# Optimization experiments

Measured on AMD Instinct MI355X. Metric: run time of the kernel, lower is better.

Reference implementation:

```python
import jax, jax.numpy as jnp
import numpy as np

N_NODES = 50000
N_EDGES = 800000
D_IN = 64
D_OUT = 64


def setup_inputs() -> dict:
    key = jax.random.key(0)
    k1, k2, k3, k4, k5 = jax.random.split(key, 5)
    x = jax.random.normal(k1, (N_NODES, D_IN), dtype=jnp.float32)
    senders = jax.random.randint(k2, (N_EDGES,), 0, N_NODES, dtype=jnp.int32)
    receivers = jax.random.randint(k3, (N_EDGES,), 0, N_NODES, dtype=jnp.int32)
    # eqx.nn.Linear params: weight [out, in], bias [out]
    weight = jax.random.normal(k4, (D_OUT, D_IN), dtype=jnp.float32) / np.sqrt(D_IN)
    bias = jax.random.normal(k5, (D_OUT,), dtype=jnp.float32) * 0.01
    return {"x": x, "senders": senders, "receivers": receivers, "weight": weight, "bias": bias}


def reference(x, senders, receivers, weight, bias):
    n = x.shape[0]
    # jraph.GraphConvolution applies update_node_fn (the Linear) FIRST
    h = x @ weight.T + bias  # [N, D_OUT]
    # add self edges
    self_idx = jnp.arange(n, dtype=senders.dtype)
    cs = jnp.concatenate([senders, self_idx])
    cr = jnp.concatenate([receivers, self_idx])
    ones = jnp.ones(cs.shape, dtype=h.dtype)
    sender_deg = jax.ops.segment_sum(ones, cs, num_segments=n)
    receiver_deg = jax.ops.segment_sum(ones, cr, num_segments=n)
    # symmetric normalization: D^{-1/2} A D^{-1/2}
    h = h * jax.lax.rsqrt(jnp.maximum(sender_deg, 1.0))[:, None]
    h = jax.ops.segment_sum(h[cs], cr, num_segments=n)  # gather -> scatter-add
    h = h * jax.lax.rsqrt(jnp.maximum(receiver_deg, 1.0))[:, None]
    return jax.nn.leaky_relu(h)  # default negative_slope=0.01
```

## Files before the change

kernel.cpp:

```cpp
#include <hip/hip_runtime.h>

#define N_NODES 50000
#define N_EDGES 800000
#define D 64
#define NB 196
#define BSZ 256
#define NSLICE 196
#define E4 (N_EDGES / 4)

__device__ __forceinline__ ushort f2bf(float f) {
    unsigned u = __float_as_uint(f);
    unsigned r = u + 0x7fffu + ((u >> 16) & 1u);
    return (ushort)(r >> 16);
}
__device__ __forceinline__ void acc8(const uint4 a, float* acc) {
    acc[0] += __uint_as_float(a.x << 16);
    acc[1] += __uint_as_float(a.x & 0xffff0000u);
    acc[2] += __uint_as_float(a.y << 16);
    acc[3] += __uint_as_float(a.y & 0xffff0000u);
    acc[4] += __uint_as_float(a.z << 16);
    acc[5] += __uint_as_float(a.z & 0xffff0000u);
    acc[6] += __uint_as_float(a.w << 16);
    acc[7] += __uint_as_float(a.w & 0xffff0000u);
}

__global__ __launch_bounds__(1024) void count_kernel(
        const int* __restrict__ s, const int* __restrict__ r,
        int* __restrict__ rcnt, int* __restrict__ scnt) {
    __shared__ int rh[NB], sh[NB];
    const int tid = threadIdx.x, sl = blockIdx.x;
    for (int i = tid; i < NB; i += 1024) { rh[i] = 0; sh[i] = 0; }
    __syncthreads();

    int e4 = sl * 1024 + tid;
    if (e4 < E4) {
        int4 rv = ((const int4*)r)[e4];
        int4 sv = ((const int4*)s)[e4];
        atomicAdd(&rh[rv.x >> 8], 1); atomicAdd(&rh[rv.y >> 8], 1);
        atomicAdd(&rh[rv.z >> 8], 1); atomicAdd(&rh[rv.w >> 8], 1);
        atomicAdd(&sh[sv.x >> 8], 1); atomicAdd(&sh[sv.y >> 8], 1);
        atomicAdd(&sh[sv.z >> 8], 1); atomicAdd(&sh[sv.w >> 8], 1);
    }
    __syncthreads();
    for (int i = tid; i < NB; i += 1024) {
        rcnt[i * NSLICE + sl] = rh[i];
        scnt[i * NSLICE + sl] = sh[i];
    }
}

__global__ __launch_bounds__(256) void scanA_kernel(
        int* __restrict__ rcnt, int* __restrict__ scnt,
        int* __restrict__ rtot, int* __restrict__ stot) {
    __shared__ int sc[256];
    const int tid = threadIdx.x;
    const int b = blockIdx.x;
    int* arr = (b < NB) ? rcnt : scnt;
    int* tot = (b < NB) ? rtot : stot;
    const int bb = (b < NB) ? b : b - NB;

    int v = (tid < NSLICE) ? arr[bb * NSLICE + tid] : 0;
    sc[tid] = v;
    __syncthreads();
    for (int o = 1; o < 256; o <<= 1) {
        int u = (tid >= o) ? sc[tid - o] : 0;
        __syncthreads();
        sc[tid] += u;
        __syncthreads();
    }
    if (tid < NSLICE) arr[bb * NSLICE + tid] = sc[tid] - v;
    if (tid == 255) tot[bb] = sc[255];
}

__global__ __launch_bounds__(1024) void part_kernel(
        const int* __restrict__ s, const int* __restrict__ r,
        const int* __restrict__ rcnt, const int* __restrict__ scnt,
        const int* __restrict__ rtot, const int* __restrict__ stot,
        unsigned* __restrict__ pr, unsigned char* __restrict__ ps8) {
    __shared__ int rcur[NB], scur[NB];
    __shared__ int sc[256];
    const int tid = threadIdx.x, sl = blockIdx.x;

    if (tid < 256) sc[tid] = (tid < NB) ? rtot[tid] : 0;
    __syncthreads();
    for (int o = 1; o < 256; o <<= 1) {
        int u = 0;
        if (tid < 256 && tid >= o) u = sc[tid - o];
        __syncthreads();
        if (tid < 256) sc[tid] += u;
        __syncthreads();
    }
    if (tid < NB) rcur[tid] = ((tid == 0) ? 0 : sc[tid - 1]) + rcnt[tid * NSLICE + sl];
    __syncthreads();
    if (tid < 256) sc[tid] = (tid < NB) ? stot[tid] : 0;
    __syncthreads();
    for (int o = 1; o < 256; o <<= 1) {
        int u = 0;
        if (tid < 256 && tid >= o) u = sc[tid - o];
        __syncthreads();
        if (tid < 256) sc[tid] += u;
        __syncthreads();
    }
    if (tid < NB) scur[tid] = ((tid == 0) ? 0 : sc[tid - 1]) + scnt[tid * NSLICE + sl];
    __syncthreads();

    int e4 = sl * 1024 + tid;
    if (e4 < E4) {
        int4 rv = ((const int4*)r)[e4];
        int4 sv = ((const int4*)s)[e4];
        int ri[4] = {rv.x, rv.y, rv.z, rv.w};
        int si[4] = {sv.x, sv.y, sv.z, sv.w};
        #pragma unroll
        for (int k = 0; k < 4; ++k) {
            int pos = atomicAdd(&rcur[ri[k] >> 8], 1);
            pr[pos] = ((unsigned)(ri[k] & 255) << 16) | (unsigned)si[k];
            int pos2 = atomicAdd(&scur[si[k] >> 8], 1);
            ps8[pos2] = (unsigned char)(si[k] & 255);
        }
    }
}

__global__ __launch_bounds__(256) void post_kernel(
        const unsigned* __restrict__ pr,
        const int* __restrict__ rtot, const int* __restrict__ stot,
        int* __restrict__ rowoff, ushort* __restrict__ csr16,
        const unsigned char* __restrict__ ps8, float* __restrict__ sscale) {
    __shared__ int sc[256];
    const int tid = threadIdx.x;

    if (blockIdx.x >= NB) {
        __shared__ int hist[BSZ];
        const int b = blockIdx.x - NB;
        sc[tid] = (tid < NB) ? stot[tid] : 0;
        __syncthreads();
        for (int o = 1; o < 256; o <<= 1) {
            int u = (tid >= o) ? sc[tid - o] : 0;
            __syncthreads();
            sc[tid] += u;
            __syncthreads();
        }
        const int sb = (b == 0) ? 0 : sc[b - 1];
        const int se = sc[b];
        hist[tid] = 0;
        __syncthreads();
        for (int i = sb + tid; i < se; i += 256) atomicAdd(&hist[ps8[i]], 1);
        __syncthreads();
        int n = b * BSZ + tid;
        if (n < N_NODES) sscale[n] = rsqrtf((float)(hist[tid] + 1));
        return;
    }
    __shared__ int hist2[BSZ];
    __shared__ int cur[BSZ];
    const int b = blockIdx.x;
    sc[tid] = (tid < NB) ? rtot[tid] : 0;
    __syncthreads();
    for (int o = 1; o < 256; o <<= 1) {
        int u = (tid >= o) ? sc[tid - o] : 0;
        __syncthreads();
        sc[tid] += u;
        __syncthreads();
    }
    const int rb = (b == 0) ? 0 : sc[b - 1];
    const int re = sc[b];

    hist2[tid] = 0;
    __syncthreads();
    for (int i = rb + tid; i < re; i += 256)
        atomicAdd(&hist2[pr[i] >> 16], 1);
    __syncthreads();

    int v = hist2[tid];
    __syncthreads();
    hist2[tid] = v;
    __syncthreads();
    for (int o = 1; o < 256; o <<= 1) {
        int u = (tid >= o) ? hist2[tid - o] : 0;
        __syncthreads();
        hist2[tid] += u;
        __syncthreads();
    }
    int excl = hist2[tid] - v;
    int n = b * BSZ + tid;
    if (n < N_NODES) rowoff[n] = rb + excl;
    cur[tid] = rb + excl;
    if (b == NB - 1 && tid == 0) rowoff[N_NODES] = N_EDGES;
    __syncthreads();

    for (int i = rb + tid; i < re; i += 256) {
        unsigned pw = pr[i];
        int pos = atomicAdd(&cur[pw >> 16], 1);
        csr16[pos] = (ushort)(pw & 0xffffu);
    }
}

__global__ __launch_bounds__(256, 4) void linear_kernel(
        const float* __restrict__ x, const float* __restrict__ w,
        const float* __restrict__ bias, const float* __restrict__ sscale,
        ushort* __restrict__ h16) {
    __shared__ float wlds[64 * 68];
    __shared__ float xlds[64 * 68];
    __shared__ float blds[64];
    __shared__ float slds[64];
    const int t = threadIdx.x;
    const int t15 = t & 15;
    const int g = t >> 4;
    const int nb = blockIdx.x * 64;

    #pragma unroll
    for (int q = 0; q < 4; ++q) {
        int idx = q * 256 + t;
        int o = idx >> 4, k4 = idx & 15;
        float4 wv = ((const float4*)w)[idx];
        *(float4*)&wlds[o * 68 + k4 * 4] = wv;
    }
    if (t < 64) {
        blds[t] = bias[t];
        int n = nb + t;
        slds[t] = (n < N_NODES) ? sscale[n] : 0.f;
    }
    #pragma unroll
    for (int q = 0; q < 4; ++q) {
        int idx = q * 256 + t;
        int nl = idx >> 4, k4 = idx & 15;
        int n = nb + nl;
        float4 xv = (n < N_NODES) ? ((const float4*)x)[n * 16 + k4]
                                  : make_float4(0.f, 0.f, 0.f, 0.f);
        *(float4*)&xlds[nl * 68 + k4 * 4] = xv;
    }
    __syncthreads();

    float acc[4][4];
    #pragma unroll
    for (int i = 0; i < 4; ++i)
        #pragma unroll
        for (int j = 0; j < 4; ++j) acc[i][j] = 0.f;

    #pragma unroll 2
    for (int k4 = 0; k4 < 16; ++k4) {
        float4 wv0 = *(const float4*)&wlds[(t15     ) * 68 + k4 * 4];
        float4 wv1 = *(const float4*)&wlds[(t15 + 16) * 68 + k4 * 4];
        float4 wv2 = *(const float4*)&wlds[(t15 + 32) * 68 + k4 * 4];
        float4 wv3 = *(const float4*)&wlds[(t15 + 48) * 68 + k4 * 4];
        #pragma unroll
        for (int i = 0; i < 4; ++i) {
            float4 xv = *(const float4*)&xlds[(g * 4 + i) * 68 + k4 * 4];
            acc[i][0] += xv.x * wv0.x + xv.y * wv0.y + xv.z * wv0.z + xv.w * wv0.w;
            acc[i][1] += xv.x * wv1.x + xv.y * wv1.y + xv.z * wv1.z + xv.w * wv1.w;
            acc[i][2] += xv.x * wv2.x + xv.y * wv2.y + xv.z * wv2.z + xv.w * wv2.w;
            acc[i][3] += xv.x * wv3.x + xv.y * wv3.y + xv.z * wv3.z + xv.w * wv3.w;
        }
    }

    #pragma unroll
    for (int i = 0; i < 4; ++i) {
        int nl = g * 4 + i;
        int n = nb + nl;
        if (n < N_NODES) {
            float sc = slds[nl];
            h16[n * D + t15     ] = f2bf((acc[i][0] + blds[t15     ]) * sc);
            h16[n * D + t15 + 16] = f2bf((acc[i][1] + blds[t15 + 16]) * sc);
            h16[n * D + t15 + 32] = f2bf((acc[i][2] + blds[t15 + 32]) * sc);
            h16[n * D + t15 + 48] = f2bf((acc[i][3] + blds[t15 + 48]) * sc);
        }
    }
}

__global__ __launch_bounds__(256) void gather_kernel(
        const ushort* __restrict__ h16, const int* __restrict__ rowoff,
        const ushort* __restrict__ csr16, float* __restrict__ out) {
    const int lane = threadIdx.x & 63;
    const int q = lane & 7;
    const int g = lane >> 3;
    const int n = blockIdx.x * 4 + (threadIdx.x >> 6);
    if (n >= N_NODES) return;

    float acc[8];
    #pragma unroll
    for (int k = 0; k < 8; ++k) acc[k] = 0.f;

    const int base = rowoff[n];
    const int cnt = rowoff[n + 1] - base;

    for (int j0 = 0; j0 < cnt; j0 += 64) {
        int m = cnt - j0; if (m > 64) m = 64;
        int my = (lane < m) ? (int)csr16[base + j0 + lane] : 0;
        int t = 0;
        for (; t + 16 <= m; t += 16) {
            int s0 = __shfl(my, t + g);
            int s1 = __shfl(my, t + 8 + g);
            uint4 a = *(const uint4*)&h16[s0 * D + q * 8];
            uint4 b = *(const uint4*)&h16[s1 * D + q * 8];
            acc8(a, acc);
            acc8(b, acc);
        }
        for (; t < m; t += 8) {
            int e = t + g;
            int ee = (e < m) ? e : 0;
            int s0 = __shfl(my, ee);
            if (e < m) {
                uint4 a = *(const uint4*)&h16[s0 * D + q * 8];
                acc8(a, acc);
            }
        }
    }

    #pragma unroll
    for (int k = 0; k < 8; ++k) acc[k] += __shfl_xor(acc[k], 8);
    #pragma unroll
    for (int k = 0; k < 8; ++k) acc[k] += __shfl_xor(acc[k], 16);
    #pragma unroll
    for (int k = 0; k < 8; ++k) acc[k] += __shfl_xor(acc[k], 32);

    uint4 sv = *(const uint4*)&h16[n * D + q * 8];
    acc8(sv, acc);
    float sc = rsqrtf((float)(cnt + 1));
    float o[8];
    #pragma unroll
    for (int k = 0; k < 8; ++k) {
        float vv = acc[k] * sc;
        o[k] = vv > 0.f ? vv : 0.01f * vv;
    }
    if (g == 0) {
        float4* op = (float4*)(out + n * D + q * 8);
        op[0] = make_float4(o[0], o[1], o[2], o[3]);
        op[1] = make_float4(o[4], o[5], o[6], o[7]);
    }
}

extern "C" void kernel_launch(void* const* d_in, const int* in_sizes, int n_in,
                              void* d_out, int out_size, void* d_ws, size_t ws_size,
                              hipStream_t stream) {
    const float* x       = (const float*)d_in[0];
    const int*   senders = (const int*)d_in[1];
    const int*   recvs   = (const int*)d_in[2];
    const float* weight  = (const float*)d_in[3];
    const float* bias    = (const float*)d_in[4];
    float* out = (float*)d_out;

    char* p = (char*)d_ws;
    auto take = [&](size_t bytes) { char* q = p; p += (bytes + 255) & ~(size_t)255; return q; };
    ushort*        h16    = (ushort*)take((size_t)N_NODES * D * 2);
    float*         sscale = (float*)take((size_t)N_NODES * 4);
    unsigned*      pr     = (unsigned*)take((size_t)N_EDGES * 4);
    unsigned char* ps8    = (unsigned char*)take((size_t)N_EDGES);
    int*           rcnt   = (int*)take((size_t)NB * NSLICE * 4);
    int*           scnt   = (int*)take((size_t)NB * NSLICE * 4);
    int*           rtot   = (int*)take((size_t)NB * 4);
    int*           stot   = (int*)take((size_t)NB * 4);
    int*           rowoff = (int*)take((size_t)(N_NODES + 1) * 4);
    ushort*        csr16  = (ushort*)take((size_t)N_EDGES * 2);

    hipLaunchKernelGGL(count_kernel, dim3(NSLICE), dim3(1024), 0, stream,
                       senders, recvs, rcnt, scnt);
    hipLaunchKernelGGL(scanA_kernel, dim3(2 * NB), dim3(256), 0, stream,
                       rcnt, scnt, rtot, stot);
    hipLaunchKernelGGL(part_kernel, dim3(NSLICE), dim3(1024), 0, stream,
                       senders, recvs, rcnt, scnt, rtot, stot, pr, ps8);
    hipLaunchKernelGGL(post_kernel, dim3(2 * NB), dim3(BSZ), 0, stream,
                       pr, rtot, stot, rowoff, csr16, ps8, sscale);
    hipLaunchKernelGGL(linear_kernel, dim3((N_NODES + 63) / 64), dim3(256), 0, stream,
                       x, weight, bias, sscale, h16);
    hipLaunchKernelGGL(gather_kernel, dim3((N_NODES + 3) / 4), dim3(256), 0, stream,
                       h16, rowoff, csr16, out);
}
```

Measured before the change: 76.92 us.

## Fuse CSR build kernels into one cooperative kernel with grid syncs

```diff
diff --git a/kernel.cpp b/kernel.cpp
--- a/kernel.cpp
+++ b/kernel.cpp
@@ -1,12 +1,17 @@
 #include <hip/hip_runtime.h>
+#include <hip/hip_cooperative_groups.h>
+
+namespace cg = cooperative_groups;
 
 #define N_NODES 50000
 #define N_EDGES 800000
 #define D 64
 #define NB 196
 #define BSZ 256
-#define NSLICE 196
-#define E4 (N_EDGES / 4)
+#define MBLK 256
+#define MTHR 1024
+#define SLICE_E 3136
+#define SLICE_I4 784
 
 __device__ __forceinline__ ushort f2bf(float f) {
     unsigned u = __float_as_uint(f);
@@ -24,61 +29,70 @@
     acc[7] += __uint_as_float(a.w & 0xffff0000u);
 }
 
-__global__ __launch_bounds__(1024) void count_kernel(
+__global__ __launch_bounds__(MTHR) void mega_kernel(
         const int* __restrict__ s, const int* __restrict__ r,
-        int* __restrict__ rcnt, int* __restrict__ scnt) {
+        int* __restrict__ rcnt, int* __restrict__ scnt,
+        int* __restrict__ rtot, int* __restrict__ stot,
+        unsigned* __restrict__ pr, unsigned char* __restrict__ ps8,
+        int* __restrict__ rowoff, ushort* __restrict__ csr16,
+        float* __restrict__ sscale) {
+    __shared__ unsigned ecache[SLICE_E];
     __shared__ int rh[NB], sh[NB];
-    const int tid = threadIdx.x, sl = blockIdx.x;
-    for (int i = tid; i < NB; i += 1024) { rh[i] = 0; sh[i] = 0; }
-    __syncthreads();
-
-    int e4 = sl * 1024 + tid;
-    if (e4 < E4) {
-        int4 rv = ((const int4*)r)[e4];
-        int4 sv = ((const int4*)s)[e4];
-        atomicAdd(&rh[rv.x >> 8], 1); atomicAdd(&rh[rv.y >> 8], 1);
-        atomicAdd(&rh[rv.z >> 8], 1); atomicAdd(&rh[rv.w >> 8], 1);
-        atomicAdd(&sh[sv.x >> 8], 1); atomicAdd(&sh[sv.y >> 8], 1);
-        atomicAdd(&sh[sv.z >> 8], 1); atomicAdd(&sh[sv.w >> 8], 1);
-    }
-    __syncthreads();
-    for (int i = tid; i < NB; i += 1024) {
-        rcnt[i * NSLICE + sl] = rh[i];
-        scnt[i * NSLICE + sl] = sh[i];
-    }
-}
-
-__global__ __launch_bounds__(256) void scanA_kernel(
-        int* __restrict__ rcnt, int* __restrict__ scnt,
-        int* __restrict__ rtot, int* __restrict__ stot) {
     __shared__ int sc[256];
+    __shared__ int h4[256];
+    __shared__ int c4[256];
+    cg::grid_group grid = cg::this_grid();
+
     const int tid = threadIdx.x;
-    const int b = blockIdx.x;
-    int* arr = (b < NB) ? rcnt : scnt;
-    int* tot = (b < NB) ? rtot : stot;
-    const int bb = (b < NB) ? b : b - NB;
-
-    int v = (tid < NSLICE) ? arr[bb * NSLICE + tid] : 0;
-    sc[tid] = v;
-    __syncthreads();
-    for (int o = 1; o < 256; o <<= 1) {
-        int u = (tid >= o) ? sc[tid - o] : 0;
-        __syncthreads();
-        sc[tid] += u;
-        __syncthreads();
-    }
-    if (tid < NSLICE) arr[bb * NSLICE + tid] = sc[tid] - v;
-    if (tid == 255) tot[bb] = sc[255];
-}
-
-__global__ __launch_bounds__(1024) void part_kernel(
-        const int* __restrict__ s, const int* __restrict__ r,
-        const int* __restrict__ rcnt, const int* __restrict__ scnt,
-        const int* __restrict__ rtot, const int* __restrict__ stot,
-        unsigned* __restrict__ pr, unsigned char* __restrict__ ps8) {
-    __shared__ int rcur[NB], scur[NB];
-    __shared__ int sc[256];
-    const int tid = threadIdx.x, sl = blockIdx.x;
+    const int sl = blockIdx.x;
+    const int ebase = sl * SLICE_E;
+    const int ecount = min(SLICE_E, N_EDGES - ebase);
+    const int i4n = (ecount + 3) >> 2;
+
+    for (int i = tid; i < NB; i += MTHR) { rh[i] = 0; sh[i] = 0; }
+    __syncthreads();
+    if (tid < i4n) {
+        int4 rv = ((const int4*)r)[sl * SLICE_I4 + tid];
+        int4 sv = ((const int4*)s)[sl * SLICE_I4 + tid];
+        int ri[4] = {rv.x, rv.y, rv.z, rv.w};
+        int si[4] = {sv.x, sv.y, sv.z, sv.w};
+        #pragma unroll
+        for (int k = 0; k < 4; ++k) {
+            atomicAdd(&rh[ri[k] >> 8], 1);
+            atomicAdd(&sh[si[k] >> 8], 1);
+            ecache[tid * 4 + k] = ((unsigned)ri[k] << 16) | (unsigned)si[k];
+        }
+    }
+    __syncthreads();
+    for (int i = tid; i < NB; i += MTHR) {
+        rcnt[i * MBLK + sl] = rh[i];
+        scnt[i * MBLK + sl] = sh[i];
+    }
+    grid.sync();
+
+    #pragma unroll
+    for (int jj = 0; jj < 2; ++jj) {
+        int job = sl + jj * MBLK;
+        if (job < 2 * NB) {
+            int* arr = (job < NB) ? rcnt : scnt;
+            int* tot = (job < NB) ? rtot : stot;
+            int bb = (job < NB) ? job : job - NB;
+            int v = 0;
+            if (tid < 256) { v = arr[bb * MBLK + tid]; sc[tid] = v; }
+            __syncthreads();
+            for (int o = 1; o < 256; o <<= 1) {
+                int u = 0;
+                if (tid < 256 && tid >= o) u = sc[tid - o];
+                __syncthreads();
+                if (tid < 256) sc[tid] += u;
+                __syncthreads();
+            }
+            if (tid < 256) arr[bb * MBLK + tid] = sc[tid] - v;
+            if (tid == 255) tot[bb] = sc[255];
+            __syncthreads();
+        }
+    }
+    grid.sync();
 
     if (tid < 256) sc[tid] = (tid < NB) ? rtot[tid] : 0;
     __syncthreads();
@@ -89,7 +103,7 @@
         if (tid < 256) sc[tid] += u;
         __syncthreads();
     }
-    if (tid < NB) rcur[tid] = ((tid == 0) ? 0 : sc[tid - 1]) + rcnt[tid * NSLICE + sl];
+    if (tid < NB) rh[tid] = ((tid == 0) ? 0 : sc[tid - 1]) + rcnt[tid * MBLK + sl];
     __syncthreads();
     if (tid < 256) sc[tid] = (tid < NB) ? stot[tid] : 0;
     __syncthreads();
@@ -100,95 +114,91 @@
         if (tid < 256) sc[tid] += u;
         __syncthreads();
     }
-    if (tid < NB) scur[tid] = ((tid == 0) ? 0 : sc[tid - 1]) + scnt[tid * NSLICE + sl];
-    __syncthreads();
-
-    int e4 = sl * 1024 + tid;
-    if (e4 < E4) {
-        int4 rv = ((const int4*)r)[e4];
-        int4 sv = ((const int4*)s)[e4];
-        int ri[4] = {rv.x, rv.y, rv.z, rv.w};
-        int si[4] = {sv.x, sv.y, sv.z, sv.w};
-        #pragma unroll
-        for (int k = 0; k < 4; ++k) {
-            int pos = atomicAdd(&rcur[ri[k] >> 8], 1);
-            pr[pos] = ((unsigned)(ri[k] & 255) << 16) | (unsigned)si[k];
-            int pos2 = atomicAdd(&scur[si[k] >> 8], 1);
-            ps8[pos2] = (unsigned char)(si[k] & 255);
-        }
-    }
-}
-
-__global__ __launch_bounds__(256) void post_kernel(
-        const unsigned* __restrict__ pr,
-        const int* __restrict__ rtot, const int* __restrict__ stot,
-        int* __restrict__ rowoff, ushort* __restrict__ csr16,
-        const unsigned char* __restrict__ ps8, float* __restrict__ sscale) {
-    __shared__ int sc[256];
-    const int tid = threadIdx.x;
-
-    if (blockIdx.x >= NB) {
-        __shared__ int hist[BSZ];
-        const int b = blockIdx.x - NB;
-        sc[tid] = (tid < NB) ? stot[tid] : 0;
-        __syncthreads();
-        for (int o = 1; o < 256; o <<= 1) {
-            int u = (tid >= o) ? sc[tid - o] : 0;
-            __syncthreads();
-            sc[tid] += u;
-            __syncthreads();
-        }
-        const int sb = (b == 0) ? 0 : sc[b - 1];
-        const int se = sc[b];
-        hist[tid] = 0;
-        __syncthreads();
-        for (int i = sb + tid; i < se; i += 256) atomicAdd(&hist[ps8[i]], 1);
-        __syncthreads();
-        int n = b * BSZ + tid;
-        if (n < N_NODES) sscale[n] = rsqrtf((float)(hist[tid] + 1));
-        return;
-    }
-    __shared__ int hist2[BSZ];
-    __shared__ int cur[BSZ];
-    const int b = blockIdx.x;
-    sc[tid] = (tid < NB) ? rtot[tid] : 0;
-    __syncthreads();
-    for (int o = 1; o < 256; o <<= 1) {
-        int u = (tid >= o) ? sc[tid - o] : 0;
-        __syncthreads();
-        sc[tid] += u;
-        __syncthreads();
-    }
-    const int rb = (b == 0) ? 0 : sc[b - 1];
-    const int re = sc[b];
-
-    hist2[tid] = 0;
-    __syncthreads();
-    for (int i = rb + tid; i < re; i += 256)
-        atomicAdd(&hist2[pr[i] >> 16], 1);
-    __syncthreads();
-
-    int v = hist2[tid];
-    __syncthreads();
-    hist2[tid] = v;
-    __syncthreads();
-    for (int o = 1; o < 256; o <<= 1) {
-        int u = (tid >= o) ? hist2[tid - o] : 0;
-        __syncthreads();
-        hist2[tid] += u;
-        __syncthreads();
-    }
-    int excl = hist2[tid] - v;
-    int n = b * BSZ + tid;
-    if (n < N_NODES) rowoff[n] = rb + excl;
-    cur[tid] = rb + excl;
-    if (b == NB - 1 && tid == 0) rowoff[N_NODES] = N_EDGES;
-    __syncthreads();
-
-    for (int i = rb + tid; i < re; i += 256) {
-        unsigned pw = pr[i];
-        int pos = atomicAdd(&cur[pw >> 16], 1);
-        csr16[pos] = (ushort)(pw & 0xffffu);
+    if (tid < NB) sh[tid] = ((tid == 0) ? 0 : sc[tid - 1]) + scnt[tid * MBLK + sl];
+    __syncthreads();
+
+    for (int e = tid; e < ecount; e += MTHR) {
+        unsigned pe = ecache[e];
+        unsigned re_ = pe >> 16, se_ = pe & 0xffffu;
+        int pos = atomicAdd(&rh[re_ >> 8], 1);
+        pr[pos] = ((re_ & 255u) << 16) | se_;
+        int pos2 = atomicAdd(&sh[se_ >> 8], 1);
+        ps8[pos2] = (unsigned char)(se_ & 255u);
+    }
+    grid.sync();
+
+    #pragma unroll
+    for (int jj = 0; jj < 2; ++jj) {
+        int job = sl + jj * MBLK;
+        if (job >= 2 * NB) continue;
+        if (job < NB) {
+            const int b = job;
+            if (tid < 256) sc[tid] = (tid < NB) ? rtot[tid] : 0;
+            __syncthreads();
+            for (int o = 1; o < 256; o <<= 1) {
+                int u = 0;
+                if (tid < 256 && tid >= o) u = sc[tid - o];
+                __syncthreads();
+                if (tid < 256) sc[tid] += u;
+                __syncthreads();
+            }
+            const int rb = (b == 0) ? 0 : sc[b - 1];
+            const int re = sc[b];
+            __syncthreads();
+            if (tid < 256) h4[tid] = 0;
+            __syncthreads();
+            for (int i = rb + tid; i < re; i += MTHR)
+                atomicAdd(&h4[pr[i] >> 16], 1);
+            __syncthreads();
+            int v = (tid < 256) ? h4[tid] : 0;
+            if (tid < 256) sc[tid] = v;
+            __syncthreads();
+            for (int o = 1; o < 256; o <<= 1) {
+                int u = 0;
+                if (tid < 256 && tid >= o) u = sc[tid - o];
+                __syncthreads();
+                if (tid < 256) sc[tid] += u;
+                __syncthreads();
+            }
+            if (tid < 256) {
+                int excl = sc[tid] - v;
+                int n = b * BSZ + tid;
+                if (n < N_NODES) rowoff[n] = rb + excl;
+                c4[tid] = rb + excl;
+            }
+            if (b == NB - 1 && tid == 0) rowoff[N_NODES] = N_EDGES;
+            __syncthreads();
+            for (int i = rb + tid; i < re; i += MTHR) {
+                unsigned pw = pr[i];
+                int pos = atomicAdd(&c4[pw >> 16], 1);
+                csr16[pos] = (ushort)(pw & 0xffffu);
+            }
+            __syncthreads();
+        } else {
+            const int b = job - NB;
+            if (tid < 256) sc[tid] = (tid < NB) ? stot[tid] : 0;
+            __syncthreads();
+            for (int o = 1; o < 256; o <<= 1) {
+                int u = 0;
+                if (tid < 256 && tid >= o) u = sc[tid - o];
+                __syncthreads();
+                if (tid < 256) sc[tid] += u;
+                __syncthreads();
+            }
+            const int sb = (b == 0) ? 0 : sc[b - 1];
+            const int se = sc[b];
+            __syncthreads();
+            if (tid < 256) h4[tid] = 0;
+            __syncthreads();
+            for (int i = sb + tid; i < se; i += MTHR)
+                atomicAdd(&h4[ps8[i]], 1);
+            __syncthreads();
+            if (tid < 256) {
+                int n = b * BSZ + tid;
+                if (n < N_NODES) sscale[n] = rsqrtf((float)(h4[tid] + 1));
+            }
+            __syncthreads();
+        }
     }
 }
 
@@ -320,9 +330,9 @@
         o[k] = vv > 0.f ? vv : 0.01f * vv;
     }
     if (g == 0) {
-        float4* op = (float4*)(out + n * D + q * 8);
-        op[0] = make_float4(o[0], o[1], o[2], o[3]);
-        op[1] = make_float4(o[4], o[5], o[6], o[7]);
+        *(float4*)(out + n * D + q * 8)     = make_float4(o[0], o[1], o[2], o[3]);
+    } else if (g == 1) {
+        *(float4*)(out + n * D + q * 8 + 4) = make_float4(o[4], o[5], o[6], o[7]);
     }
 }
 
@@ -342,21 +352,21 @@
     float*         sscale = (float*)take((size_t)N_NODES * 4);
     unsigned*      pr     = (unsigned*)take((size_t)N_EDGES * 4);
     unsigned char* ps8    = (unsigned char*)take((size_t)N_EDGES);
-    int*           rcnt   = (int*)take((size_t)NB * NSLICE * 4);
-    int*           scnt   = (int*)take((size_t)NB * NSLICE * 4);
+    int*           rcnt   = (int*)take((size_t)NB * MBLK * 4);
+    int*           scnt   = (int*)take((size_t)NB * MBLK * 4);
     int*           rtot   = (int*)take((size_t)NB * 4);
     int*           stot   = (int*)take((size_t)NB * 4);
     int*           rowoff = (int*)take((size_t)(N_NODES + 1) * 4);
     ushort*        csr16  = (ushort*)take((size_t)N_EDGES * 2);
 
-    hipLaunchKernelGGL(count_kernel, dim3(NSLICE), dim3(1024), 0, stream,
-                       senders, recvs, rcnt, scnt);
-    hipLaunchKernelGGL(scanA_kernel, dim3(2 * NB), dim3(256), 0, stream,
-                       rcnt, scnt, rtot, stot);
-    hipLaunchKernelGGL(part_kernel, dim3(NSLICE), dim3(1024), 0, stream,
-                       senders, recvs, rcnt, scnt, rtot, stot, pr, ps8);
-    hipLaunchKernelGGL(post_kernel, dim3(2 * NB), dim3(BSZ), 0, stream,
-                       pr, rtot, stot, rowoff, csr16, ps8, sscale);
+    {
+        const int* s_ = senders; const int* r_ = recvs;
+        void* args[] = {(void*)&s_, (void*)&r_, (void*)&rcnt, (void*)&scnt,
+                        (void*)&rtot, (void*)&stot, (void*)&pr, (void*)&ps8,
+                        (void*)&rowoff, (void*)&csr16, (void*)&sscale};
+        hipLaunchCooperativeKernel((const void*)mega_kernel, dim3(MBLK), dim3(MTHR),
+                                   args, 0, stream);
+    }
     hipLaunchKernelGGL(linear_kernel, dim3((N_NODES + 63) / 64), dim3(256), 0, stream,
                        x, weight, bias, sscale, h16);
     hipLaunchKernelGGL(gather_kernel, dim3((N_NODES + 3) / 4), dim3(256), 0, stream,
```

Result: slower. 179.5 us (+133.4%).

## Bucket edges into fixed-capacity per-slice cells, dropping count and scan passes

Applied to the files above, without the earlier changes.

```diff
diff --git a/kernel.cpp b/kernel.cpp
--- a/kernel.cpp
+++ b/kernel.cpp
@@ -7,6 +7,7 @@
 #define BSZ 256
 #define NSLICE 196
 #define E4 (N_EDGES / 4)
+#define CAP 64
 
 __device__ __forceinline__ ushort f2bf(float f) {
     unsigned u = __float_as_uint(f);
@@ -24,85 +25,16 @@
     acc[7] += __uint_as_float(a.w & 0xffff0000u);
 }
 
-__global__ __launch_bounds__(1024) void count_kernel(
+__global__ __launch_bounds__(1024) void part1_kernel(
         const int* __restrict__ s, const int* __restrict__ r,
+        unsigned* __restrict__ prc, unsigned char* __restrict__ psc,
         int* __restrict__ rcnt, int* __restrict__ scnt) {
-    __shared__ int rh[NB], sh[NB];
+    __shared__ int rcur[NB], scur[NB];
     const int tid = threadIdx.x, sl = blockIdx.x;
-    for (int i = tid; i < NB; i += 1024) { rh[i] = 0; sh[i] = 0; }
-    __syncthreads();
-
-    int e4 = sl * 1024 + tid;
-    if (e4 < E4) {
-        int4 rv = ((const int4*)r)[e4];
-        int4 sv = ((const int4*)s)[e4];
-        atomicAdd(&rh[rv.x >> 8], 1); atomicAdd(&rh[rv.y >> 8], 1);
-        atomicAdd(&rh[rv.z >> 8], 1); atomicAdd(&rh[rv.w >> 8], 1);
-        atomicAdd(&sh[sv.x >> 8], 1); atomicAdd(&sh[sv.y >> 8], 1);
-        atomicAdd(&sh[sv.z >> 8], 1); atomicAdd(&sh[sv.w >> 8], 1);
-    }
-    __syncthreads();
-    for (int i = tid; i < NB; i += 1024) {
-        rcnt[i * NSLICE + sl] = rh[i];
-        scnt[i * NSLICE + sl] = sh[i];
-    }
-}
-
-__global__ __launch_bounds__(256) void scanA_kernel(
-        int* __restrict__ rcnt, int* __restrict__ scnt,
-        int* __restrict__ rtot, int* __restrict__ stot) {
-    __shared__ int sc[256];
-    const int tid = threadIdx.x;
-    const int b = blockIdx.x;
-    int* arr = (b < NB) ? rcnt : scnt;
-    int* tot = (b < NB) ? rtot : stot;
-    const int bb = (b < NB) ? b : b - NB;
-
-    int v = (tid < NSLICE) ? arr[bb * NSLICE + tid] : 0;
-    sc[tid] = v;
-    __syncthreads();
-    for (int o = 1; o < 256; o <<= 1) {
-        int u = (tid >= o) ? sc[tid - o] : 0;
-        __syncthreads();
-        sc[tid] += u;
-        __syncthreads();
-    }
-    if (tid < NSLICE) arr[bb * NSLICE + tid] = sc[tid] - v;
-    if (tid == 255) tot[bb] = sc[255];
-}
-
-__global__ __launch_bounds__(1024) void part_kernel(
-        const int* __restrict__ s, const int* __restrict__ r,
-        const int* __restrict__ rcnt, const int* __restrict__ scnt,
-        const int* __restrict__ rtot, const int* __restrict__ stot,
-        unsigned* __restrict__ pr, unsigned char* __restrict__ ps8) {
-    __shared__ int rcur[NB], scur[NB];
-    __shared__ int sc[256];
-    const int tid = threadIdx.x, sl = blockIdx.x;
-
-    if (tid < 256) sc[tid] = (tid < NB) ? rtot[tid] : 0;
-    __syncthreads();
-    for (int o = 1; o < 256; o <<= 1) {
-        int u = 0;
-        if (tid < 256 && tid >= o) u = sc[tid - o];
-        __syncthreads();
-        if (tid < 256) sc[tid] += u;
-        __syncthreads();
-    }
-    if (tid < NB) rcur[tid] = ((tid == 0) ? 0 : sc[tid - 1]) + rcnt[tid * NSLICE + sl];
-    __syncthreads();
-    if (tid < 256) sc[tid] = (tid < NB) ? stot[tid] : 0;
-    __syncthreads();
-    for (int o = 1; o < 256; o <<= 1) {
-        int u = 0;
-        if (tid < 256 && tid >= o) u = sc[tid - o];
-        __syncthreads();
-        if (tid < 256) sc[tid] += u;
-        __syncthreads();
-    }
-    if (tid < NB) scur[tid] = ((tid == 0) ? 0 : sc[tid - 1]) + scnt[tid * NSLICE + sl];
-    __syncthreads();
-
+    for (int i = tid; i < NB; i += 1024) { rcur[i] = 0; scur[i] = 0; }
+    __syncthreads();
+
+    const size_t cellbase = (size_t)sl * NB * CAP;
     int e4 = sl * 1024 + tid;
     if (e4 < E4) {
         int4 rv = ((const int4*)r)[e4];
@@ -111,47 +43,54 @@
         int si[4] = {sv.x, sv.y, sv.z, sv.w};
         #pragma unroll
         for (int k = 0; k < 4; ++k) {
-            int pos = atomicAdd(&rcur[ri[k] >> 8], 1);
-            pr[pos] = ((unsigned)(ri[k] & 255) << 16) | (unsigned)si[k];
-            int pos2 = atomicAdd(&scur[si[k] >> 8], 1);
-            ps8[pos2] = (unsigned char)(si[k] & 255);
-        }
+            int b = ri[k] >> 8;
+            int pos = atomicAdd(&rcur[b], 1);
+            if (pos < CAP)
+                prc[cellbase + (size_t)b * CAP + pos] =
+                    ((unsigned)(ri[k] & 255) << 16) | (unsigned)si[k];
+            int bs = si[k] >> 8;
+            int pos2 = atomicAdd(&scur[bs], 1);
+            if (pos2 < CAP)
+                psc[cellbase + (size_t)bs * CAP + pos2] = (unsigned char)(si[k] & 255);
+        }
+    }
+    __syncthreads();
+    for (int i = tid; i < NB; i += 1024) {
+        rcnt[sl * NB + i] = rcur[i];
+        scnt[sl * NB + i] = scur[i];
     }
 }
 
 __global__ __launch_bounds__(256) void post_kernel(
-        const unsigned* __restrict__ pr,
-        const int* __restrict__ rtot, const int* __restrict__ stot,
+        const unsigned* __restrict__ prc, const unsigned char* __restrict__ psc,
+        const int* __restrict__ rcnt, const int* __restrict__ scnt,
         int* __restrict__ rowoff, ushort* __restrict__ csr16,
-        const unsigned char* __restrict__ ps8, float* __restrict__ sscale) {
+        float* __restrict__ sscale) {
     __shared__ int sc[256];
+    __shared__ int h4[BSZ];
     const int tid = threadIdx.x;
 
     if (blockIdx.x >= NB) {
-        __shared__ int hist[BSZ];
         const int b = blockIdx.x - NB;
-        sc[tid] = (tid < NB) ? stot[tid] : 0;
-        __syncthreads();
-        for (int o = 1; o < 256; o <<= 1) {
-            int u = (tid >= o) ? sc[tid - o] : 0;
-            __syncthreads();
-            sc[tid] += u;
-            __syncthreads();
-        }
-        const int sb = (b == 0) ? 0 : sc[b - 1];
-        const int se = sc[b];
-        hist[tid] = 0;
-        __syncthreads();
-        for (int i = sb + tid; i < se; i += 256) atomicAdd(&hist[ps8[i]], 1);
+        h4[tid] = 0;
+        __syncthreads();
+        for (int sl = tid; sl < NSLICE; sl += 256) {
+            int c = scnt[sl * NB + b];
+            const unsigned char* cell = psc + (size_t)sl * NB * CAP + (size_t)b * CAP;
+            for (int i = 0; i < c; ++i) atomicAdd(&h4[cell[i]], 1);
+        }
         __syncthreads();
         int n = b * BSZ + tid;
-        if (n < N_NODES) sscale[n] = rsqrtf((float)(hist[tid] + 1));
+        if (n < N_NODES) sscale[n] = rsqrtf((float)(h4[tid] + 1));
         return;
     }
-    __shared__ int hist2[BSZ];
-    __shared__ int cur[BSZ];
+
     const int b = blockIdx.x;
-    sc[tid] = (tid < NB) ? rtot[tid] : 0;
+    int tot = 0;
+    if (tid < NB) {
+        for (int sl = 0; sl < NSLICE; ++sl) tot += rcnt[sl * NB + tid];
+    }
+    sc[tid] = tot;
     __syncthreads();
     for (int o = 1; o < 256; o <<= 1) {
         int u = (tid >= o) ? sc[tid - o] : 0;
@@ -160,35 +99,41 @@
         __syncthreads();
     }
     const int rb = (b == 0) ? 0 : sc[b - 1];
-    const int re = sc[b];
-
-    hist2[tid] = 0;
-    __syncthreads();
-    for (int i = rb + tid; i < re; i += 256)
-        atomicAdd(&hist2[pr[i] >> 16], 1);
-    __syncthreads();
-
-    int v = hist2[tid];
-    __syncthreads();
-    hist2[tid] = v;
+    __syncthreads();
+
+    h4[tid] = 0;
+    __syncthreads();
+    for (int sl = tid; sl < NSLICE; sl += 256) {
+        int c = rcnt[sl * NB + b];
+        const unsigned* cell = prc + (size_t)sl * NB * CAP + (size_t)b * CAP;
+        for (int i = 0; i < c; ++i) atomicAdd(&h4[cell[i] >> 16], 1);
+    }
+    __syncthreads();
+
+    int v = h4[tid];
+    sc[tid] = v;
     __syncthreads();
     for (int o = 1; o < 256; o <<= 1) {
-        int u = (tid >= o) ? hist2[tid - o] : 0;
-        __syncthreads();
-        hist2[tid] += u;
-        __syncthreads();
-    }
-    int excl = hist2[tid] - v;
+        int u = (tid >= o) ? sc[tid - o] : 0;
+        __syncthreads();
+        sc[tid] += u;
+        __syncthreads();
+    }
+    int excl = sc[tid] - v;
     int n = b * BSZ + tid;
     if (n < N_NODES) rowoff[n] = rb + excl;
-    cur[tid] = rb + excl;
+    h4[tid] = rb + excl;
     if (b == NB - 1 && tid == 0) rowoff[N_NODES] = N_EDGES;
     __syncthreads();
 
-    for (int i = rb + tid; i < re; i += 256) {
-        unsigned pw = pr[i];
-        int pos = atomicAdd(&cur[pw >> 16], 1);
-        csr16[pos] = (ushort)(pw & 0xffffu);
+    for (int sl = tid; sl < NSLICE; sl += 256) {
+        int c = rcnt[sl * NB + b];
+        const unsigned* cell = prc + (size_t)sl * NB * CAP + (size_t)b * CAP;
+        for (int i = 0; i < c; ++i) {
+            unsigned pw = cell[i];
+            int pos = atomicAdd(&h4[pw >> 16], 1);
+            csr16[pos] = (ushort)(pw & 0xffffu);
+        }
     }
 }
 
@@ -320,9 +265,9 @@
         o[k] = vv > 0.f ? vv : 0.01f * vv;
     }
     if (g == 0) {
-        float4* op = (float4*)(out + n * D + q * 8);
-        op[0] = make_float4(o[0], o[1], o[2], o[3]);
-        op[1] = make_float4(o[4], o[5], o[6], o[7]);
+        *(float4*)(out + n * D + q * 8)     = make_float4(o[0], o[1], o[2], o[3]);
+    } else if (g == 1) {
+        *(float4*)(out + n * D + q * 8 + 4) = make_float4(o[4], o[5], o[6], o[7]);
     }
 }
 
@@ -340,23 +285,17 @@
     auto take = [&](size_t bytes) { char* q = p; p += (bytes + 255) & ~(size_t)255; return q; };
     ushort*        h16    = (ushort*)take((size_t)N_NODES * D * 2);
     float*         sscale = (float*)take((size_t)N_NODES * 4);
-    unsigned*      pr     = (unsigned*)take((size_t)N_EDGES * 4);
-    unsigned char* ps8    = (unsigned char*)take((size_t)N_EDGES);
-    int*           rcnt   = (int*)take((size_t)NB * NSLICE * 4);
-    int*           scnt   = (int*)take((size_t)NB * NSLICE * 4);
-    int*           rtot   = (int*)take((size_t)NB * 4);
-    int*           stot   = (int*)take((size_t)NB * 4);
+    unsigned*      prc    = (unsigned*)take((size_t)NSLICE * NB * CAP * 4);
+    unsigned char* psc    = (unsigned char*)take((size_t)NSLICE * NB * CAP);
+    int*           rcnt   = (int*)take((size_t)NSLICE * NB * 4);
+    int*           scnt   = (int*)take((size_t)NSLICE * NB * 4);
     int*           rowoff = (int*)take((size_t)(N_NODES + 1) * 4);
     ushort*        csr16  = (ushort*)take((size_t)N_EDGES * 2);
 
-    hipLaunchKernelGGL(count_kernel, dim3(NSLICE), dim3(1024), 0, stream,
-                       senders, recvs, rcnt, scnt);
-    hipLaunchKernelGGL(scanA_kernel, dim3(2 * NB), dim3(256), 0, stream,
-                       rcnt, scnt, rtot, stot);
-    hipLaunchKernelGGL(part_kernel, dim3(NSLICE), dim3(1024), 0, stream,
-                       senders, recvs, rcnt, scnt, rtot, stot, pr, ps8);
+    hipLaunchKernelGGL(part1_kernel, dim3(NSLICE), dim3(1024), 0, stream,
+                       senders, recvs, prc, psc, rcnt, scnt);
     hipLaunchKernelGGL(post_kernel, dim3(2 * NB), dim3(BSZ), 0, stream,
-                       pr, rtot, stot, rowoff, csr16, ps8, sscale);
+                       prc, psc, rcnt, scnt, rowoff, csr16, sscale);
     hipLaunchKernelGGL(linear_kernel, dim3((N_NODES + 63) / 64), dim3(256), 0, stream,
                        x, weight, bias, sscale, h16);
     hipLaunchKernelGGL(gather_kernel, dim3((N_NODES + 3) / 4), dim3(256), 0, stream,
```

Result: faster. 68.92 us (-10.4%).
